# Performance work log

Measured on AMD Instinct MI355X. Metric: run time of the kernel, lower is better.

Reference implementation:

```python
import jax, jax.numpy as jnp
import numpy as np

NUM_NODES = 100000
NUM_EDGES = 600000
NUM_GRAPHS = 512
D = 128  # num_features == latent widths


def setup_inputs() -> dict:
    key = jax.random.key(0)
    ks = jax.random.split(key, 16)
    inp = {
        "x": jax.random.normal(ks[0], (NUM_NODES, D), dtype=jnp.float32),
        "edge_index": jax.random.randint(ks[1], (2, NUM_EDGES), 0, NUM_NODES, dtype=jnp.int32),
        "batch": jnp.sort(jax.random.randint(ks[2], (NUM_NODES,), 0, NUM_GRAPHS, dtype=jnp.int32)),
    }
    s = 1.0 / np.sqrt(D)
    # SAGEConv params per layer: lin_l (applied to mean-aggregated neighbors), lin_r (root), bias
    for i in range(3):
        inp[f"Wl{i+1}"] = jax.random.uniform(ks[3 + 3 * i], (D, D), jnp.float32, -s, s)
        inp[f"Wr{i+1}"] = jax.random.uniform(ks[4 + 3 * i], (D, D), jnp.float32, -s, s)
        inp[f"b{i+1}"] = jax.random.uniform(ks[5 + 3 * i], (D,), jnp.float32, -s, s)
    inp["Wro"] = jax.random.uniform(ks[12], (D, 1), jnp.float32, -s, s)
    inp["bro"] = jax.random.uniform(ks[13], (1,), jnp.float32, -s, s)
    return inp


def _sage_conv(h, Wl, Wr, b, src, dst):
    # mean aggregation of source features at destination nodes
    msg = jax.ops.segment_sum(h[src], dst, num_segments=NUM_NODES)          # [N, D]
    cnt = jax.ops.segment_sum(jnp.ones((src.shape[0], 1), h.dtype), dst,
                              num_segments=NUM_NODES)                        # [N, 1]
    mean = msg / jnp.maximum(cnt, 1.0)
    return mean @ Wl + h @ Wr + b


def reference(x, edge_index, batch, Wl1, Wr1, b1, Wl2, Wr2, b2, Wl3, Wr3, b3, Wro, bro):
    src, dst = edge_index[0], edge_index[1]
    h = x
    for Wl, Wr, b in ((Wl1, Wr1, b1), (Wl2, Wr2, b2), (Wl3, Wr3, b3)):
        h = jax.nn.relu(_sage_conv(h, Wl, Wr, b, src, dst))
    # per-graph sum pooling (replaces the python loop over unique batch ids)
    pooled = jax.ops.segment_sum(h, batch, num_segments=NUM_GRAPHS)  # [G, D]
    return jax.nn.sigmoid(pooled @ Wro + bro)  # [G, 1]
```

## Files before the change

### kernel.cpp

```cpp
#include <hip/hip_runtime.h>
#include <math.h>

#define N_NODES 100000
#define N_EDGES 600000
#define N_GRAPHS 512
#define D 128
#define SCAN_BS 1024
#define SCAN_NBC ((N_NODES + SCAN_BS - 1) / SCAN_BS)
#define NPART 8
#define PART_SZ (N_NODES / NPART)
#define E4 (N_EDGES / 4)

typedef unsigned short u16;
typedef __attribute__((ext_vector_type(8))) short short8;
typedef __attribute__((ext_vector_type(4))) float f32x4;

__device__ __forceinline__ u16 f2bf(float f) {
    unsigned int u = __float_as_uint(f);
    u += 0x7FFFu + ((u >> 16) & 1u);
    return (u16)(u >> 16);
}
__device__ __forceinline__ float bf2f(u16 h) {
    return __uint_as_float(((unsigned int)h) << 16);
}
__device__ __forceinline__ void split2(float f, unsigned int& h16, unsigned int& l16) {
    unsigned int u = __float_as_uint(f);
    unsigned int hb = (u + (0x7FFFu + ((u >> 16) & 1u))) & 0xffff0000u;
    float lo = f - __uint_as_float(hb);
    unsigned int ul = __float_as_uint(lo);
    h16 = hb >> 16;
    l16 = (ul + (0x7FFFu + ((ul >> 16) & 1u))) >> 16;
}

typedef __attribute__((address_space(1))) const unsigned int gas_u32;
typedef __attribute__((address_space(3))) unsigned int las_u32;
__device__ __forceinline__ void gload16(const void* g, void* l) {
    __builtin_amdgcn_global_load_lds((gas_u32*)g, (las_u32*)l, 16, 0, 0);
}

__global__ __launch_bounds__(256) void zero_i_kernel(int* __restrict__ p, int n) {
    int i = blockIdx.x * 256 + threadIdx.x;
    if (i < n) p[i] = 0;
}

__global__ __launch_bounds__(256) void hist_kernel(const int* __restrict__ dst,
                                                   int* __restrict__ deg) {
    const int lo = (blockIdx.x & (NPART - 1)) * PART_SZ;
    const int i4 = (blockIdx.x >> 3) * 256 + threadIdx.x;
    if (i4 >= E4) return;
    const int4 d4 = ((const int4*)dst)[i4];
    if ((unsigned)(d4.x - lo) < (unsigned)PART_SZ) atomicAdd(&deg[d4.x], 1);
    if ((unsigned)(d4.y - lo) < (unsigned)PART_SZ) atomicAdd(&deg[d4.y], 1);
    if ((unsigned)(d4.z - lo) < (unsigned)PART_SZ) atomicAdd(&deg[d4.z], 1);
    if ((unsigned)(d4.w - lo) < (unsigned)PART_SZ) atomicAdd(&deg[d4.w], 1);
}

__global__ __launch_bounds__(1024) void scan1_kernel(const int* __restrict__ deg,
                                                     int* __restrict__ excl,
                                                     int* __restrict__ blocksum) {
    __shared__ int buf[2][SCAN_BS];
    const int t = threadIdx.x;
    const int gid = blockIdx.x * SCAN_BS + t;
    int v = (gid < N_NODES) ? deg[gid] : 0;
    buf[0][t] = v;
    __syncthreads();
    int pi = 0;
    for (int off = 1; off < SCAN_BS; off <<= 1) {
        int val = buf[pi][t];
        if (t >= off) val += buf[pi][t - off];
        buf[pi ^ 1][t] = val;
        pi ^= 1;
        __syncthreads();
    }
    int incl = buf[pi][t];
    if (gid < N_NODES) excl[gid] = incl - v;
    if (t == SCAN_BS - 1) blocksum[blockIdx.x] = incl;
}

__global__ __launch_bounds__(256) void scan3_kernel(const int* __restrict__ excl,
                                                    const int* __restrict__ blocksum,
                                                    int* __restrict__ rowptr) {
    __shared__ int buf[2][128];
    const int t = threadIdx.x;
    if (t < 128) buf[0][t] = (t < SCAN_NBC) ? blocksum[t] : 0;
    __syncthreads();
    int pi = 0;
    for (int off = 1; off < 128; off <<= 1) {
        if (t < 128) {
            int val = buf[pi][t];
            if (t >= off) val += buf[pi][t - off];
            buf[pi ^ 1][t] = val;
        }
        pi ^= 1;
        __syncthreads();
    }
    const int i = blockIdx.x * 256 + t;
    if (i < N_NODES) {
        const int j = i / SCAN_BS;
        const int pref = (j == 0) ? 0 : buf[pi][j - 1];
        rowptr[i] = excl[i] + pref;
    }
    if (i == 0) rowptr[N_NODES] = N_EDGES;
}

__global__ __launch_bounds__(256) void fill_kernel(const int* __restrict__ src,
                                                   const int* __restrict__ dst,
                                                   const int* __restrict__ rowptr,
                                                   int* __restrict__ fill,
                                                   int* __restrict__ csr_src) {
    const int lo = (blockIdx.x & (NPART - 1)) * PART_SZ;
    const int i4 = (blockIdx.x >> 3) * 256 + threadIdx.x;
    if (i4 >= E4) return;
    const int4 d4 = ((const int4*)dst)[i4];
    const int4 s4 = ((const int4*)src)[i4];
    if ((unsigned)(d4.x - lo) < (unsigned)PART_SZ) {
        int pos = rowptr[d4.x] + atomicAdd(&fill[d4.x], 1);
        csr_src[pos] = s4.x;
    }
    if ((unsigned)(d4.y - lo) < (unsigned)PART_SZ) {
        int pos = rowptr[d4.y] + atomicAdd(&fill[d4.y], 1);
        csr_src[pos] = s4.y;
    }
    if ((unsigned)(d4.z - lo) < (unsigned)PART_SZ) {
        int pos = rowptr[d4.z] + atomicAdd(&fill[d4.z], 1);
        csr_src[pos] = s4.z;
    }
    if ((unsigned)(d4.w - lo) < (unsigned)PART_SZ) {
        int pos = rowptr[d4.w] + atomicAdd(&fill[d4.w], 1);
        csr_src[pos] = s4.w;
    }
}

__global__ __launch_bounds__(256) void split_x_kernel(const float* __restrict__ x,
                                                      u16* __restrict__ Hhi,
                                                      u16* __restrict__ Hlo) {
    const int i = blockIdx.x * 256 + threadIdx.x;
    const float4 v = ((const float4*)x)[i];
    unsigned int h0, l0, h1, l1, h2, l2, h3, l3;
    split2(v.x, h0, l0); split2(v.y, h1, l1);
    split2(v.z, h2, l2); split2(v.w, h3, l3);
    uint2 oh, ol;
    oh.x = h0 | (h1 << 16); oh.y = h2 | (h3 << 16);
    ol.x = l0 | (l1 << 16); ol.y = l2 | (l3 << 16);
    ((uint2*)Hhi)[i] = oh;
    ((uint2*)Hlo)[i] = ol;
}

__global__ __launch_bounds__(64) void wprep_kernel(const float* __restrict__ Wl1, const float* __restrict__ Wr1,
                                                   const float* __restrict__ Wl2, const float* __restrict__ Wr2,
                                                   const float* __restrict__ Wl3, const float* __restrict__ Wr3,
                                                   u16* __restrict__ wph, u16* __restrict__ wpl) {
    const int layer = blockIdx.x >> 6;
    const int t = blockIdx.x & 63;
    const int lane = threadIdx.x;
    const float* Wl = (layer == 0) ? Wl1 : (layer == 1) ? Wl2 : Wl3;
    const float* Wr = (layer == 0) ? Wr1 : (layer == 1) ? Wr2 : Wr3;
    const int nt = t >> 3, kt = t & 7;
    const int n = nt * 16 + (lane & 15);
    const int k0 = kt * 32 + (lane >> 4) * 8;
    const size_t base = (size_t)layer * 32768 + (size_t)(t * 64 + lane) * 8;
    #pragma unroll
    for (int j = 0; j < 8; ++j) {
        const int k = k0 + j;
        const float w = (k < 128) ? Wl[k * 128 + n] : Wr[(k - 128) * 128 + n];
        const u16 h = f2bf(w);
        wph[base + j] = h;
        wpl[base + j] = f2bf(w - bf2f(h));
    }
}

__global__ __launch_bounds__(256) void agg_kernel(const u16* __restrict__ Hhi,
                                                  const int* __restrict__ rowptr,
                                                  const int* __restrict__ csr_src,
                                                  u16* __restrict__ Mb) {
    const int lane = threadIdx.x & 63;
    const int node = blockIdx.x * 4 + (threadIdx.x >> 6);
    if (node >= N_NODES) return;
    const int beg = rowptr[node];
    const int end = rowptr[node + 1];
    const unsigned int* H32 = (const unsigned int*)Hhi;
    float a0 = 0.f, a1 = 0.f;

    for (int c0 = beg; c0 < end; c0 += 64) {
        const int nv = min(64, end - c0);
        int msrc = (c0 + lane < end) ? csr_src[c0 + lane] : 0;
        int j = 0;
        for (; j + 8 <= nv; j += 8) {
            const int s0 = __shfl(msrc, j + 0);
            const int s1 = __shfl(msrc, j + 1);
            const int s2 = __shfl(msrc, j + 2);
            const int s3 = __shfl(msrc, j + 3);
            const int s4 = __shfl(msrc, j + 4);
            const int s5 = __shfl(msrc, j + 5);
            const int s6 = __shfl(msrc, j + 6);
            const int s7 = __shfl(msrc, j + 7);
            const unsigned int w0 = H32[(size_t)s0 * 64 + lane];
            const unsigned int w1 = H32[(size_t)s1 * 64 + lane];
            const unsigned int w2 = H32[(size_t)s2 * 64 + lane];
            const unsigned int w3 = H32[(size_t)s3 * 64 + lane];
            const unsigned int w4 = H32[(size_t)s4 * 64 + lane];
            const unsigned int w5 = H32[(size_t)s5 * 64 + lane];
            const unsigned int w6 = H32[(size_t)s6 * 64 + lane];
            const unsigned int w7 = H32[(size_t)s7 * 64 + lane];
            a0 += __uint_as_float(w0 << 16) + __uint_as_float(w1 << 16)
                + __uint_as_float(w2 << 16) + __uint_as_float(w3 << 16)
                + __uint_as_float(w4 << 16) + __uint_as_float(w5 << 16)
                + __uint_as_float(w6 << 16) + __uint_as_float(w7 << 16);
            a1 += __uint_as_float(w0 & 0xffff0000u) + __uint_as_float(w1 & 0xffff0000u)
                + __uint_as_float(w2 & 0xffff0000u) + __uint_as_float(w3 & 0xffff0000u)
                + __uint_as_float(w4 & 0xffff0000u) + __uint_as_float(w5 & 0xffff0000u)
                + __uint_as_float(w6 & 0xffff0000u) + __uint_as_float(w7 & 0xffff0000u);
        }
        for (; j + 4 <= nv; j += 4) {
            const int s0 = __shfl(msrc, j + 0);
            const int s1 = __shfl(msrc, j + 1);
            const int s2 = __shfl(msrc, j + 2);
            const int s3 = __shfl(msrc, j + 3);
            const unsigned int w0 = H32[(size_t)s0 * 64 + lane];
            const unsigned int w1 = H32[(size_t)s1 * 64 + lane];
            const unsigned int w2 = H32[(size_t)s2 * 64 + lane];
            const unsigned int w3 = H32[(size_t)s3 * 64 + lane];
            a0 += __uint_as_float(w0 << 16) + __uint_as_float(w1 << 16)
                + __uint_as_float(w2 << 16) + __uint_as_float(w3 << 16);
            a1 += __uint_as_float(w0 & 0xffff0000u) + __uint_as_float(w1 & 0xffff0000u)
                + __uint_as_float(w2 & 0xffff0000u) + __uint_as_float(w3 & 0xffff0000u);
        }
        for (; j < nv; ++j) {
            const int s = __shfl(msrc, j);
            const unsigned int w = H32[(size_t)s * 64 + lane];
            a0 += __uint_as_float(w << 16);
            a1 += __uint_as_float(w & 0xffff0000u);
        }
    }
    const float inv = 1.0f / (float)max(end - beg, 1);
    const unsigned int o = (unsigned int)f2bf(a0 * inv) | ((unsigned int)f2bf(a1 * inv) << 16);
    ((unsigned int*)Mb)[(size_t)node * 64 + lane] = o;
}

__global__ __launch_bounds__(512, 4) void gemm_kernel(const u16* __restrict__ Mb,
                                                      const u16* Hhi, const u16* Hlo,
                                                      const u16* __restrict__ Wph,
                                                      const u16* __restrict__ Wpl,
                                                      const float* __restrict__ bias,
                                                      u16* OHhi, u16* OHlo,
                                                      const float* __restrict__ Wro,
                                                      float* rowdot) {
    __shared__ uint4 ldsAll[5120];
    const int t = threadIdx.x;
    const int lane = t & 63;
    const int wv = t >> 6;
    const int m0 = blockIdx.x * 128 + wv * 16;
    int rm = m0 + (lane & 15);
    if (rm >= N_NODES) rm = 0;
    const int ko = (lane >> 4) * 8;

    short8 am[4], ah[4], al[4];
    #pragma unroll
    for (int kt = 0; kt < 4; ++kt) {
        am[kt] = *(const short8*)(Mb  + (size_t)rm * D + kt * 32 + ko);
        ah[kt] = *(const short8*)(Hhi + (size_t)rm * D + kt * 32 + ko);
        al[kt] = *(const short8*)(Hlo + (size_t)rm * D + kt * 32 + ko);
    }

    const int cl = lane & 15;
    const int g4 = (lane >> 4) << 2;
    char* bounceB = (char*)ldsAll + 65536 + wv * 2048;

    f32x4 acc8[2][4];

#define STAGE_W(Q, B) do {                                                      \
        const uint4* gh_ = (const uint4*)Wph + (Q) * 1024;                      \
        const uint4* gl_ = (const uint4*)Wpl + (Q) * 1024;                      \
        _Pragma("unroll")                                                       \
        for (int i_ = 0; i_ < 2; ++i_) {                                        \
            gload16(gh_ + t + 512 * i_,                                         \
                    (void*)&ldsAll[(B) * 2048 + wv * 64 + 512 * i_]);           \
            gload16(gl_ + t + 512 * i_,                                         \
                    (void*)&ldsAll[(B) * 2048 + 1024 + wv * 64 + 512 * i_]);    \
        }                                                                       \
    } while (0)

#define COMPUTE_S(Q, B) do {                                                    \
        const u16* bufU_ = (const u16*)(ldsAll + (B) * 2048);                   \
        _Pragma("unroll")                                                       \
        for (int l_ = 0; l_ < 2; ++l_) {                                        \
            f32x4 acc_ = {0.f, 0.f, 0.f, 0.f};                                  \
            _Pragma("unroll")                                                   \
            for (int kt_ = 0; kt_ < 8; ++kt_) {                                 \
                const int fo_ = (l_ * 8 + kt_) * 512 + lane * 8;                \
                const short8 bh_ = *(const short8*)(bufU_ + fo_);               \
                const short8 bl_ = *(const short8*)(bufU_ + 8192 + fo_);        \
                if (kt_ < 4) {                                                  \
                    acc_ = __builtin_amdgcn_mfma_f32_16x16x32_bf16(am[kt_], bh_, acc_, 0, 0, 0); \
                    acc_ = __builtin_amdgcn_mfma_f32_16x16x32_bf16(am[kt_], bl_, acc_, 0, 0, 0); \
                } else {                                                        \
                    acc_ = __builtin_amdgcn_mfma_f32_16x16x32_bf16(ah[kt_ - 4], bh_, acc_, 0, 0, 0); \
                    acc_ = __builtin_amdgcn_mfma_f32_16x16x32_bf16(ah[kt_ - 4], bl_, acc_, 0, 0, 0); \
                    acc_ = __builtin_amdgcn_mfma_f32_16x16x32_bf16(al[kt_ - 4], bh_, acc_, 0, 0, 0); \
                }                                                               \
            }                                                                   \
            acc8[(Q) >> 1][((Q) & 1) * 2 + l_] = acc_;                          \
        }                                                                       \
    } while (0)

    STAGE_W(0, 0);
    __builtin_amdgcn_sched_barrier(0);
    STAGE_W(1, 1);
    asm volatile("s_waitcnt vmcnt(4)" ::: "memory");
    __builtin_amdgcn_s_barrier();
    COMPUTE_S(0, 0);
    __builtin_amdgcn_s_barrier();
    STAGE_W(2, 0);
    asm volatile("s_waitcnt vmcnt(4)" ::: "memory");
    __builtin_amdgcn_s_barrier();
    COMPUTE_S(1, 1);
    __builtin_amdgcn_s_barrier();
    STAGE_W(3, 1);
    asm volatile("s_waitcnt vmcnt(4)" ::: "memory");
    __builtin_amdgcn_s_barrier();
    COMPUTE_S(2, 0);
    asm volatile("s_waitcnt vmcnt(0)" ::: "memory");
    __builtin_amdgcn_s_barrier();
    COMPUTE_S(3, 1);

    if (rowdot) {
        float wsum[4] = {0.f, 0.f, 0.f, 0.f};
        #pragma unroll
        for (int si = 0; si < 2; ++si) {
            #pragma unroll
            for (int nt2 = 0; nt2 < 4; ++nt2) {
                const int col = (si * 4 + nt2) * 16 + cl;
                const float bv = bias[col];
                const float wroc = Wro[col];
                #pragma unroll
                for (int r = 0; r < 4; ++r) {
                    const float v = fmaxf(acc8[si][nt2][r] + bv, 0.f);
                    wsum[r] = fmaf(v, wroc, wsum[r]);
                }
            }
        }
        #pragma unroll
        for (int r = 0; r < 4; ++r) {
            float tsum = wsum[r];
            tsum += __shfl_down(tsum, 8, 64);
            tsum += __shfl_down(tsum, 4, 64);
            tsum += __shfl_down(tsum, 2, 64);
            tsum += __shfl_down(tsum, 1, 64);
            const int row = m0 + g4 + r;
            if (cl == 0 && row < N_NODES) {
                rowdot[row] = tsum;
            }
        }
    } else {
        #pragma unroll
        for (int si = 0; si < 2; ++si) {
            asm volatile("s_waitcnt lgkmcnt(0)" ::: "memory");
            unsigned int lo_pack[8];
            #pragma unroll
            for (int nt2 = 0; nt2 < 4; ++nt2) {
                const int col = (si * 4 + nt2) * 16 + cl;
                const float bv = bias[col];
                #pragma unroll
                for (int r = 0; r < 4; ++r) {
                    const int row16 = g4 + r;
                    const float v = fmaxf(acc8[si][nt2][r] + bv, 0.f);
                    unsigned int h16, l16;
                    split2(v, h16, l16);
                    const int boff = (row16 * 128 + (nt2 * 16 + cl) * 2) ^ ((row16 & 7) << 4);
                    *(u16*)(bounceB + boff) = (u16)h16;
                    if (r & 1) lo_pack[nt2 * 2 + (r >> 1)] |= l16 << 16;
                    else       lo_pack[nt2 * 2 + (r >> 1)]  = l16;
                }
            }
            asm volatile("s_waitcnt lgkmcnt(0)" ::: "memory");
            #pragma unroll
            for (int j = 0; j < 2; ++j) {
                const int row16 = j * 8 + (lane >> 3);
                const int blk = lane & 7;
                const uint4 vv = *(const uint4*)(bounceB + row16 * 128 + ((blk ^ (row16 & 7)) << 4));
                const int grow = blockIdx.x * 128 + wv * 16 + row16;
                if (grow < N_NODES)
                    *(uint4*)(OHhi + (size_t)grow * D + si * 64 + blk * 8) = vv;
            }
            asm volatile("s_waitcnt lgkmcnt(0)" ::: "memory");
            #pragma unroll
            for (int nt2 = 0; nt2 < 4; ++nt2) {
                #pragma unroll
                for (int r = 0; r < 4; ++r) {
                    const int row16 = g4 + r;
                    const unsigned int l16 = (lo_pack[nt2 * 2 + (r >> 1)] >> ((r & 1) * 16)) & 0xffffu;
                    const int boff = (row16 * 128 + (nt2 * 16 + cl) * 2) ^ ((row16 & 7) << 4);
                    *(u16*)(bounceB + boff) = (u16)l16;
                }
            }
            asm volatile("s_waitcnt lgkmcnt(0)" ::: "memory");
            #pragma unroll
            for (int j = 0; j < 2; ++j) {
                const int row16 = j * 8 + (lane >> 3);
                const int blk = lane & 7;
                const uint4 vv = *(const uint4*)(bounceB + row16 * 128 + ((blk ^ (row16 & 7)) << 4));
                const int grow = blockIdx.x * 128 + wv * 16 + row16;
                if (grow < N_NODES)
                    *(uint4*)(OHlo + (size_t)grow * D + si * 64 + blk * 8) = vv;
            }
        }
    }
#undef STAGE_W
#undef COMPUTE_S
}

__global__ __launch_bounds__(64) void final_kernel(const float* __restrict__ rowdot,
                                                   const int* __restrict__ batch,
                                                   const float* __restrict__ bro,
                                                   float* __restrict__ out) {
    const int g = blockIdx.x;
    const int t = threadIdx.x;
    int lo = 0, hi = N_NODES;
    while (lo < hi) { int mid = (lo + hi) >> 1; if (batch[mid] < g) lo = mid + 1; else hi = mid; }
    int lo2 = lo, hi2 = N_NODES;
    while (lo2 < hi2) { int mid = (lo2 + hi2) >> 1; if (batch[mid] < g + 1) lo2 = mid + 1; else hi2 = mid; }

    float acc = 0.0f;
    for (int i = lo + t; i < lo2; i += 64) acc += rowdot[i];
    #pragma unroll
    for (int off = 32; off > 0; off >>= 1) acc += __shfl_down(acc, off, 64);
    if (t == 0) out[g] = 1.0f / (1.0f + expf(-(acc + bro[0])));
}

extern "C" void kernel_launch(void* const* d_in, const int* in_sizes, int n_in,
                              void* d_out, int out_size, void* d_ws, size_t ws_size,
                              hipStream_t stream) {
    const float* x     = (const float*)d_in[0];
    const int*   ei    = (const int*)d_in[1];
    const int*   batch = (const int*)d_in[2];
    const int*   src   = ei;
    const int*   dst   = ei + N_EDGES;
    const float* Wl[3] = {(const float*)d_in[3], (const float*)d_in[6], (const float*)d_in[9]};
    const float* Wr[3] = {(const float*)d_in[4], (const float*)d_in[7], (const float*)d_in[10]};
    const float* bs[3] = {(const float*)d_in[5], (const float*)d_in[8], (const float*)d_in[11]};
    const float* Wro   = (const float*)d_in[12];
    const float* bro   = (const float*)d_in[13];
    float* out = (float*)d_out;

    const size_t ND = (size_t)N_NODES * D;
    char* ws = (char*)d_ws;
    u16* Hhi = (u16*)ws;
    u16* Hlo = Hhi + ND;
    u16* Mb  = Hlo + ND;
    u16* Wph = Mb + ND;
    u16* Wpl = Wph + 3 * 32768;
    int* deg      = (int*)(Wpl + 3 * 32768);
    int* fill     = deg + N_NODES;
    float* rowdot = (float*)(fill + N_NODES);
    int* excl     = (int*)(rowdot + N_NODES);
    int* blocksum = excl + N_NODES;
    int* rowptr   = blocksum + 128;
    int* csr_src  = rowptr + N_NODES + 1;

    const int NB      = (N_NODES + 255) / 256;
    const int NB2     = (2 * N_NODES + 255) / 256;
    const int EPB     = ((E4 + 255) / 256) * NPART;
    const int SPLIT_B = (int)(ND / 4 / 256);
    const int AGG_B   = N_NODES / 4;
    const int GEMM_B  = (N_NODES + 127) / 128;

    zero_i_kernel<<<NB2, 256, 0, stream>>>(deg, 2 * N_NODES);
    hist_kernel<<<EPB, 256, 0, stream>>>(dst, deg);
    scan1_kernel<<<SCAN_NBC, SCAN_BS, 0, stream>>>(deg, excl, blocksum);
    scan3_kernel<<<NB, 256, 0, stream>>>(excl, blocksum, rowptr);
    fill_kernel<<<EPB, 256, 0, stream>>>(src, dst, rowptr, fill, csr_src);

    split_x_kernel<<<SPLIT_B, 256, 0, stream>>>(x, Hhi, Hlo);
    wprep_kernel<<<192, 64, 0, stream>>>(Wl[0], Wr[0], Wl[1], Wr[1], Wl[2], Wr[2], Wph, Wpl);

    for (int l = 0; l < 3; ++l) {
        float* rdl = (l == 2) ? rowdot : (float*)nullptr;
        agg_kernel<<<AGG_B, 256, 0, stream>>>(Hhi, rowptr, csr_src, Mb);
        gemm_kernel<<<GEMM_B, 512, 0, stream>>>(Mb, Hhi, Hlo,
                                                Wph + l * 32768, Wpl + l * 32768, bs[l],
                                                Hhi, Hlo, Wro, rdl);
    }

    final_kernel<<<N_GRAPHS, 64, 0, stream>>>(rowdot, batch, bro, out);
}
```

Baseline: 385.3 us.

## Widen aggregation gathers to 8-byte loads with half-wave edge split; merge prep kernels

```diff
diff --git a/kernel.cpp b/kernel.cpp
--- a/kernel.cpp
+++ b/kernel.cpp
@@ -10,6 +10,7 @@
 #define NPART 8
 #define PART_SZ (N_NODES / NPART)
 #define E4 (N_EDGES / 4)
+#define SPLIT_B 12500
 
 typedef unsigned short u16;
 typedef __attribute__((ext_vector_type(8))) short short8;
@@ -45,14 +46,8 @@
 
 __global__ __launch_bounds__(256) void hist_kernel(const int* __restrict__ dst,
                                                    int* __restrict__ deg) {
-    const int lo = (blockIdx.x & (NPART - 1)) * PART_SZ;
-    const int i4 = (blockIdx.x >> 3) * 256 + threadIdx.x;
-    if (i4 >= E4) return;
-    const int4 d4 = ((const int4*)dst)[i4];
-    if ((unsigned)(d4.x - lo) < (unsigned)PART_SZ) atomicAdd(&deg[d4.x], 1);
-    if ((unsigned)(d4.y - lo) < (unsigned)PART_SZ) atomicAdd(&deg[d4.y], 1);
-    if ((unsigned)(d4.z - lo) < (unsigned)PART_SZ) atomicAdd(&deg[d4.z], 1);
-    if ((unsigned)(d4.w - lo) < (unsigned)PART_SZ) atomicAdd(&deg[d4.w], 1);
+    int e = blockIdx.x * 256 + threadIdx.x;
+    if (e < N_EDGES) atomicAdd(&deg[dst[e]], 1);
 }
 
 __global__ __launch_bounds__(1024) void scan1_kernel(const int* __restrict__ deg,
@@ -131,41 +126,43 @@
     }
 }
 
-__global__ __launch_bounds__(256) void split_x_kernel(const float* __restrict__ x,
-                                                      u16* __restrict__ Hhi,
-                                                      u16* __restrict__ Hlo) {
-    const int i = blockIdx.x * 256 + threadIdx.x;
-    const float4 v = ((const float4*)x)[i];
-    unsigned int h0, l0, h1, l1, h2, l2, h3, l3;
-    split2(v.x, h0, l0); split2(v.y, h1, l1);
-    split2(v.z, h2, l2); split2(v.w, h3, l3);
-    uint2 oh, ol;
-    oh.x = h0 | (h1 << 16); oh.y = h2 | (h3 << 16);
-    ol.x = l0 | (l1 << 16); ol.y = l2 | (l3 << 16);
-    ((uint2*)Hhi)[i] = oh;
-    ((uint2*)Hlo)[i] = ol;
-}
-
-__global__ __launch_bounds__(64) void wprep_kernel(const float* __restrict__ Wl1, const float* __restrict__ Wr1,
+__global__ __launch_bounds__(256) void prep_kernel(const float* __restrict__ x,
+                                                   u16* __restrict__ Hhi,
+                                                   u16* __restrict__ Hlo,
+                                                   const float* __restrict__ Wl1, const float* __restrict__ Wr1,
                                                    const float* __restrict__ Wl2, const float* __restrict__ Wr2,
                                                    const float* __restrict__ Wl3, const float* __restrict__ Wr3,
                                                    u16* __restrict__ wph, u16* __restrict__ wpl) {
-    const int layer = blockIdx.x >> 6;
-    const int t = blockIdx.x & 63;
-    const int lane = threadIdx.x;
-    const float* Wl = (layer == 0) ? Wl1 : (layer == 1) ? Wl2 : Wl3;
-    const float* Wr = (layer == 0) ? Wr1 : (layer == 1) ? Wr2 : Wr3;
-    const int nt = t >> 3, kt = t & 7;
-    const int n = nt * 16 + (lane & 15);
-    const int k0 = kt * 32 + (lane >> 4) * 8;
-    const size_t base = (size_t)layer * 32768 + (size_t)(t * 64 + lane) * 8;
-    #pragma unroll
-    for (int j = 0; j < 8; ++j) {
-        const int k = k0 + j;
-        const float w = (k < 128) ? Wl[k * 128 + n] : Wr[(k - 128) * 128 + n];
-        const u16 h = f2bf(w);
-        wph[base + j] = h;
-        wpl[base + j] = f2bf(w - bf2f(h));
+    if (blockIdx.x < SPLIT_B) {
+        const int i = blockIdx.x * 256 + threadIdx.x;
+        const float4 v = ((const float4*)x)[i];
+        unsigned int h0, l0, h1, l1, h2, l2, h3, l3;
+        split2(v.x, h0, l0); split2(v.y, h1, l1);
+        split2(v.z, h2, l2); split2(v.w, h3, l3);
+        uint2 oh, ol;
+        oh.x = h0 | (h1 << 16); oh.y = h2 | (h3 << 16);
+        ol.x = l0 | (l1 << 16); ol.y = l2 | (l3 << 16);
+        ((uint2*)Hhi)[i] = oh;
+        ((uint2*)Hlo)[i] = ol;
+    } else {
+        const int b = (blockIdx.x - SPLIT_B) * 4 + (threadIdx.x >> 6);
+        const int lane = threadIdx.x & 63;
+        const int layer = b >> 6;
+        const int t = b & 63;
+        const float* Wl = (layer == 0) ? Wl1 : (layer == 1) ? Wl2 : Wl3;
+        const float* Wr = (layer == 0) ? Wr1 : (layer == 1) ? Wr2 : Wr3;
+        const int nt = t >> 3, kt = t & 7;
+        const int n = nt * 16 + (lane & 15);
+        const int k0 = kt * 32 + (lane >> 4) * 8;
+        const size_t base = (size_t)layer * 32768 + (size_t)(t * 64 + lane) * 8;
+        #pragma unroll
+        for (int j = 0; j < 8; ++j) {
+            const int k = k0 + j;
+            const float w = (k < 128) ? Wl[k * 128 + n] : Wr[(k - 128) * 128 + n];
+            const u16 h = f2bf(w);
+            wph[base + j] = h;
+            wpl[base + j] = f2bf(w - bf2f(h));
+        }
     }
 }
 
@@ -174,67 +171,67 @@
                                                   const int* __restrict__ csr_src,
                                                   u16* __restrict__ Mb) {
     const int lane = threadIdx.x & 63;
+    const int half = lane >> 5;
+    const int q = lane & 31;
     const int node = blockIdx.x * 4 + (threadIdx.x >> 6);
     if (node >= N_NODES) return;
     const int beg = rowptr[node];
     const int end = rowptr[node + 1];
-    const unsigned int* H32 = (const unsigned int*)Hhi;
-    float a0 = 0.f, a1 = 0.f;
+    const uint2* H64 = (const uint2*)Hhi;
+    float a0 = 0.f, a1 = 0.f, a2 = 0.f, a3 = 0.f;
 
     for (int c0 = beg; c0 < end; c0 += 64) {
         const int nv = min(64, end - c0);
         int msrc = (c0 + lane < end) ? csr_src[c0 + lane] : 0;
         int j = 0;
         for (; j + 8 <= nv; j += 8) {
-            const int s0 = __shfl(msrc, j + 0);
-            const int s1 = __shfl(msrc, j + 1);
-            const int s2 = __shfl(msrc, j + 2);
-            const int s3 = __shfl(msrc, j + 3);
-            const int s4 = __shfl(msrc, j + 4);
-            const int s5 = __shfl(msrc, j + 5);
-            const int s6 = __shfl(msrc, j + 6);
-            const int s7 = __shfl(msrc, j + 7);
-            const unsigned int w0 = H32[(size_t)s0 * 64 + lane];
-            const unsigned int w1 = H32[(size_t)s1 * 64 + lane];
-            const unsigned int w2 = H32[(size_t)s2 * 64 + lane];
-            const unsigned int w3 = H32[(size_t)s3 * 64 + lane];
-            const unsigned int w4 = H32[(size_t)s4 * 64 + lane];
-            const unsigned int w5 = H32[(size_t)s5 * 64 + lane];
-            const unsigned int w6 = H32[(size_t)s6 * 64 + lane];
-            const unsigned int w7 = H32[(size_t)s7 * 64 + lane];
-            a0 += __uint_as_float(w0 << 16) + __uint_as_float(w1 << 16)
-                + __uint_as_float(w2 << 16) + __uint_as_float(w3 << 16)
-                + __uint_as_float(w4 << 16) + __uint_as_float(w5 << 16)
-                + __uint_as_float(w6 << 16) + __uint_as_float(w7 << 16);
-            a1 += __uint_as_float(w0 & 0xffff0000u) + __uint_as_float(w1 & 0xffff0000u)
-                + __uint_as_float(w2 & 0xffff0000u) + __uint_as_float(w3 & 0xffff0000u)
-                + __uint_as_float(w4 & 0xffff0000u) + __uint_as_float(w5 & 0xffff0000u)
-                + __uint_as_float(w6 & 0xffff0000u) + __uint_as_float(w7 & 0xffff0000u);
-        }
-        for (; j + 4 <= nv; j += 4) {
-            const int s0 = __shfl(msrc, j + 0);
-            const int s1 = __shfl(msrc, j + 1);
-            const int s2 = __shfl(msrc, j + 2);
-            const int s3 = __shfl(msrc, j + 3);
-            const unsigned int w0 = H32[(size_t)s0 * 64 + lane];
-            const unsigned int w1 = H32[(size_t)s1 * 64 + lane];
-            const unsigned int w2 = H32[(size_t)s2 * 64 + lane];
-            const unsigned int w3 = H32[(size_t)s3 * 64 + lane];
-            a0 += __uint_as_float(w0 << 16) + __uint_as_float(w1 << 16)
-                + __uint_as_float(w2 << 16) + __uint_as_float(w3 << 16);
-            a1 += __uint_as_float(w0 & 0xffff0000u) + __uint_as_float(w1 & 0xffff0000u)
-                + __uint_as_float(w2 & 0xffff0000u) + __uint_as_float(w3 & 0xffff0000u);
-        }
-        for (; j < nv; ++j) {
+            const int t0 = __shfl(msrc, j + 0 + half);
+            const int t1 = __shfl(msrc, j + 2 + half);
+            const int t2 = __shfl(msrc, j + 4 + half);
+            const int t3 = __shfl(msrc, j + 6 + half);
+            const uint2 w0 = H64[(size_t)t0 * 32 + q];
+            const uint2 w1 = H64[(size_t)t1 * 32 + q];
+            const uint2 w2 = H64[(size_t)t2 * 32 + q];
+            const uint2 w3 = H64[(size_t)t3 * 32 + q];
+            a0 += __uint_as_float(w0.x << 16) + __uint_as_float(w1.x << 16)
+                + __uint_as_float(w2.x << 16) + __uint_as_float(w3.x << 16);
+            a1 += __uint_as_float(w0.x & 0xffff0000u) + __uint_as_float(w1.x & 0xffff0000u)
+                + __uint_as_float(w2.x & 0xffff0000u) + __uint_as_float(w3.x & 0xffff0000u);
+            a2 += __uint_as_float(w0.y << 16) + __uint_as_float(w1.y << 16)
+                + __uint_as_float(w2.y << 16) + __uint_as_float(w3.y << 16);
+            a3 += __uint_as_float(w0.y & 0xffff0000u) + __uint_as_float(w1.y & 0xffff0000u)
+                + __uint_as_float(w2.y & 0xffff0000u) + __uint_as_float(w3.y & 0xffff0000u);
+        }
+        for (; j + 2 <= nv; j += 2) {
+            const int s = __shfl(msrc, j + half);
+            const uint2 w = H64[(size_t)s * 32 + q];
+            a0 += __uint_as_float(w.x << 16);
+            a1 += __uint_as_float(w.x & 0xffff0000u);
+            a2 += __uint_as_float(w.y << 16);
+            a3 += __uint_as_float(w.y & 0xffff0000u);
+        }
+        if (j < nv) {
             const int s = __shfl(msrc, j);
-            const unsigned int w = H32[(size_t)s * 64 + lane];
-            a0 += __uint_as_float(w << 16);
-            a1 += __uint_as_float(w & 0xffff0000u);
-        }
-    }
-    const float inv = 1.0f / (float)max(end - beg, 1);
-    const unsigned int o = (unsigned int)f2bf(a0 * inv) | ((unsigned int)f2bf(a1 * inv) << 16);
-    ((unsigned int*)Mb)[(size_t)node * 64 + lane] = o;
+            if (half == 0) {
+                const uint2 w = H64[(size_t)s * 32 + q];
+                a0 += __uint_as_float(w.x << 16);
+                a1 += __uint_as_float(w.x & 0xffff0000u);
+                a2 += __uint_as_float(w.y << 16);
+                a3 += __uint_as_float(w.y & 0xffff0000u);
+            }
+        }
+    }
+    a0 += __shfl_xor(a0, 32, 64);
+    a1 += __shfl_xor(a1, 32, 64);
+    a2 += __shfl_xor(a2, 32, 64);
+    a3 += __shfl_xor(a3, 32, 64);
+    if (half == 0) {
+        const float inv = 1.0f / (float)max(end - beg, 1);
+        uint2 o;
+        o.x = (unsigned int)f2bf(a0 * inv) | ((unsigned int)f2bf(a1 * inv) << 16);
+        o.y = (unsigned int)f2bf(a2 * inv) | ((unsigned int)f2bf(a3 * inv) << 16);
+        ((uint2*)Mb)[(size_t)node * 32 + q] = o;
+    }
 }
 
 __global__ __launch_bounds__(512, 4) void gemm_kernel(const u16* __restrict__ Mb,
@@ -457,21 +454,23 @@
     int* rowptr   = blocksum + 128;
     int* csr_src  = rowptr + N_NODES + 1;
 
+    const int EB      = (N_EDGES + 255) / 256;
     const int NB      = (N_NODES + 255) / 256;
     const int NB2     = (2 * N_NODES + 255) / 256;
     const int EPB     = ((E4 + 255) / 256) * NPART;
-    const int SPLIT_B = (int)(ND / 4 / 256);
+    const int PREP_B  = SPLIT_B + 48;
     const int AGG_B   = N_NODES / 4;
     const int GEMM_B  = (N_NODES + 127) / 128;
 
     zero_i_kernel<<<NB2, 256, 0, stream>>>(deg, 2 * N_NODES);
-    hist_kernel<<<EPB, 256, 0, stream>>>(dst, deg);
+    hist_kernel<<<EB, 256, 0, stream>>>(dst, deg);
     scan1_kernel<<<SCAN_NBC, SCAN_BS, 0, stream>>>(deg, excl, blocksum);
     scan3_kernel<<<NB, 256, 0, stream>>>(excl, blocksum, rowptr);
     fill_kernel<<<EPB, 256, 0, stream>>>(src, dst, rowptr, fill, csr_src);
 
-    split_x_kernel<<<SPLIT_B, 256, 0, stream>>>(x, Hhi, Hlo);
-    wprep_kernel<<<192, 64, 0, stream>>>(Wl[0], Wr[0], Wl[1], Wr[1], Wl[2], Wr[2], Wph, Wpl);
+    prep_kernel<<<PREP_B, 256, 0, stream>>>(x, Hhi, Hlo,
+                                            Wl[0], Wr[0], Wl[1], Wr[1], Wl[2], Wr[2],
+                                            Wph, Wpl);
 
     for (int l = 0; l < 3; ++l) {
         float* rdl = (l == 2) ? rowdot : (float*)nullptr;
```

Result: no change. 384.2 us (-0.3%).
